# Kernel tuning notes

Measured on AMD Instinct MI355X. Metric: run time of the kernel, lower is better.

Reference implementation:

```python
import jax, jax.numpy as jnp
import numpy as np
from itertools import product

_EPS = 1e-5
N_VOX = 120000
C = 64
B, D, H, Wd = 2, 400, 400, 40  # batch and spatial voxel grid


def _build_rulebook(seed=0):
    """Random unique active voxels + [N,27] submanifold neighbor index table (-1 = inactive)."""
    rng = np.random.default_rng(seed)
    size = B * D * H * Wd
    flat = rng.choice(size, size=N_VOX, replace=False)
    b = flat // (D * H * Wd)
    rem = flat % (D * H * Wd)
    z = rem // (H * Wd)
    rem2 = rem % (H * Wd)
    y = rem2 // Wd
    x = rem2 % Wd
    lut = np.full(size, -1, np.int32)
    lut[flat] = np.arange(N_VOX, dtype=np.int32)
    offs = np.array(list(product([-1, 0, 1], repeat=3)), dtype=np.int64)  # [27,3]
    zz = z[:, None] + offs[None, :, 0]
    yy = y[:, None] + offs[None, :, 1]
    xx = x[:, None] + offs[None, :, 2]
    valid = (zz >= 0) & (zz < D) & (yy >= 0) & (yy < H) & (xx >= 0) & (xx < Wd)
    nf = ((b[:, None] * D + zz) * H + yy) * Wd + xx
    nbr = np.where(valid, lut[np.clip(nf, 0, size - 1)], -1).astype(np.int32)
    return nbr


def setup_inputs() -> dict:
    key = jax.random.key(0)
    ks = jax.random.split(key, 12)
    nbr = jnp.asarray(_build_rulebook())
    return {
        "features": jax.random.normal(ks[0], (N_VOX, C), jnp.float32),
        "W1": jax.random.normal(ks[1], (27, C, C), jnp.float32) * 0.05,
        "g1": jax.random.uniform(ks[2], (C,), jnp.float32, 0.5, 1.5),
        "b1": jax.random.normal(ks[3], (C,), jnp.float32) * 0.1,
        "m1": jax.random.normal(ks[4], (C,), jnp.float32) * 0.1,
        "v1": jax.random.uniform(ks[5], (C,), jnp.float32, 0.5, 1.5),
        "W2": jax.random.normal(ks[6], (27, C, C), jnp.float32) * 0.05,
        "g2": jax.random.uniform(ks[7], (C,), jnp.float32, 0.5, 1.5),
        "b2": jax.random.normal(ks[8], (C,), jnp.float32) * 0.1,
        "m2": jax.random.normal(ks[9], (C,), jnp.float32) * 0.1,
        "v2": jax.random.uniform(ks[10], (C,), jnp.float32, 0.5, 1.5),
        "nbr_idx": nbr,
    }


def _subm_conv(f, nbr, W):
    # gather-GEMM: f [N,Cin], nbr [N,27], W [27,Cin,Cout] -> [N,Cout]
    mask = (nbr >= 0)[:, :, None]
    g = jnp.where(mask, f[jnp.clip(nbr, 0)], jnp.zeros((), f.dtype))  # [N,27,Cin]
    return jnp.einsum('nkc,kcd->nd', g, W)


def _bn(x, g, b, m, v):
    return (x - m) * (g * jax.lax.rsqrt(v + _EPS)) + b


def reference(features, W1, g1, b1, m1, v1, W2, g2, b2, m2, v2, nbr_idx):
    out = _bn(_subm_conv(features, nbr_idx, W1), g1, b1, m1, v1)
    out = jax.nn.relu(out)
    out = _bn(_subm_conv(out, nbr_idx, W2), g2, b2, m2, v2)
    return jax.nn.relu(out + features)
```

## Files before the change

kernel.cpp:

```cpp
#include <hip/hip_runtime.h>

typedef short short8 __attribute__((ext_vector_type(8)));
typedef float f32x4 __attribute__((ext_vector_type(4)));

#define N_VOX 120000
#define C64 64
#define K27 27
#define KC 13
#define TILES 3750
#define CAPT 64
#define LAYER_W 110592
#define CSRB 938
#define PACKB 65
#define FUSEB 938

#define WS_TCNT 0
#define WS_BNP  16384
#define WS_PWC  20480
#define WS_PWT  40960
#define WS_ENTS 524288
#define WS_MIDB (4u << 20)

__device__ __forceinline__ ushort f2bf(float x) {
    uint u = __float_as_uint(x);
    u = (u + 0x7FFFu + ((u >> 16) & 1u)) >> 16;
    return (ushort)u;
}
__device__ __forceinline__ float bf2f(ushort u) {
    return __uint_as_float((uint)u << 16);
}

__global__ __launch_bounds__(256) void prep_csr_kernel(
    const int* __restrict__ nbr,
    const float* __restrict__ W1, const float* __restrict__ W2,
    const float* g1, const float* b1, const float* m1, const float* v1,
    const float* g2, const float* b2, const float* m2, const float* v2,
    int* __restrict__ tcnt, int2* __restrict__ ents,
    ushort* __restrict__ pwt, ushort* __restrict__ pwc,
    float* __restrict__ bnp) {
    if (blockIdx.x < CSRB) {
        __shared__ int cnt_[4];
        const int wv = threadIdx.x >> 6, lane = threadIdx.x & 63;
        const int tile = blockIdx.x * 4 + wv;
        const bool act = tile < TILES;
        if (lane == 0) cnt_[wv] = 0;
        __syncthreads();
        if (act) {
            const int base = tile * (32 * K27);
            for (int e = lane; e < 32 * K27; e += 64) {
                const int k = e % K27;
                if (k == KC) continue;
                const int m = nbr[base + e];
                if (m >= 0) {
                    const int nl = e / K27;
                    int slot = atomicAdd(&cnt_[wv], 1);
                    if (slot < CAPT) ents[tile * CAPT + slot] = make_int2(nl | (k << 8), m);
                }
            }
        }
        __syncthreads();
        if (act && lane == 0) {
            int c = cnt_[wv];
            tcnt[tile] = c > CAPT ? CAPT : c;
        }
    } else {
        int idx = (blockIdx.x - CSRB) * 256 + threadIdx.x;
        const int stride = PACKB * 256;
        for (; idx < 229440; idx += stride) {
            if (idx < 221184) {
                int L = idx / LAYER_W, r = idx % LAYER_W;
                int k = r >> 12, dc = r & 4095, d = dc >> 6, c = dc & 63;
                const float* W = L ? W2 : W1;
                pwt[idx] = f2bf(W[(size_t)k * 4096 + c * 64 + d]);
            } else if (idx < 229376) {
                int j2 = idx - 221184;
                int L = j2 >> 12, q = j2 & 4095;
                int ks = q >> 11, tq = (q >> 9) & 3, ln = (q >> 3) & 63, jj = q & 7;
                int c = ks * 32 + (ln >> 4) * 8 + jj;
                int d = tq * 16 + (ln & 15);
                const float* W = L ? W2 : W1;
                pwc[L * 4096 + q] = f2bf(W[(size_t)KC * 4096 + c * 64 + d]);
            } else {
                int i = idx - 229376;
                float s1 = g1[i] * rsqrtf(v1[i] + 1e-5f);
                bnp[i] = s1; bnp[64 + i] = b1[i] - m1[i] * s1;
                float s2 = g2[i] * rsqrtf(v2[i] + 1e-5f);
                bnp[128 + i] = s2; bnp[192 + i] = b2[i] - m2[i] * s2;
            }
        }
    }
}

template <bool L2P>
__device__ __forceinline__ void fused_core(const float* __restrict__ f,
                                           const ushort* __restrict__ midin,
                                           const ushort* __restrict__ pwc,
                                           const ushort* __restrict__ pwt,
                                           const int* __restrict__ tcnt,
                                           const int2* __restrict__ ents,
                                           const float* __restrict__ bnp,
                                           ushort* __restrict__ midout,
                                           float* __restrict__ fout,
                                           float* exw, int tile) {
    const int lane = threadIdx.x & 63;
    const int r16 = lane & 15, kg = lane >> 4;
    const int n0 = tile * 32;

#pragma unroll
    for (int i = 0; i < 8; ++i) ((f32x4*)exw)[i * 64 + lane] = (f32x4)0.f;

    const short8* B = (const short8*)pwc;
    short8 Bf[2][4];
#pragma unroll
    for (int s = 0; s < 2; ++s)
#pragma unroll
        for (int t = 0; t < 4; ++t) Bf[s][t] = B[(s * 4 + t) * 64 + lane];

    f32x4 acc[2][4];
#pragma unroll
    for (int v = 0; v < 2; ++v)
#pragma unroll
        for (int t = 0; t < 4; ++t) acc[v][t] = (f32x4)0.f;

#pragma unroll
    for (int v = 0; v < 2; ++v) {
        short8 a0, a1;
        if (L2P) {
            const short8* ar = (const short8*)(midin + (size_t)(n0 + v * 16 + r16) * C64);
            a0 = ar[kg];
            a1 = ar[4 + kg];
        } else {
            const float4* ar = (const float4*)(f + (size_t)(n0 + v * 16 + r16) * C64);
            float4 fa = ar[kg * 2], fb = ar[kg * 2 + 1];
            float4 fc = ar[8 + kg * 2], fd = ar[9 + kg * 2];
            a0[0] = f2bf(fa.x); a0[1] = f2bf(fa.y); a0[2] = f2bf(fa.z); a0[3] = f2bf(fa.w);
            a0[4] = f2bf(fb.x); a0[5] = f2bf(fb.y); a0[6] = f2bf(fb.z); a0[7] = f2bf(fb.w);
            a1[0] = f2bf(fc.x); a1[1] = f2bf(fc.y); a1[2] = f2bf(fc.z); a1[3] = f2bf(fc.w);
            a1[4] = f2bf(fd.x); a1[5] = f2bf(fd.y); a1[6] = f2bf(fd.z); a1[7] = f2bf(fd.w);
        }
#pragma unroll
        for (int t = 0; t < 4; ++t) {
            acc[v][t] = __builtin_amdgcn_mfma_f32_16x16x32_bf16(a0, Bf[0][t], acc[v][t], 0, 0, 0);
            acc[v][t] = __builtin_amdgcn_mfma_f32_16x16x32_bf16(a1, Bf[1][t], acc[v][t], 0, 0, 0);
        }
    }

    const int cnt = tcnt[tile];
    for (int p = 0; p < cnt; ++p) {
        int2 e = ents[tile * CAPT + p];
        const int ex = __builtin_amdgcn_readfirstlane(e.x);
        const int m  = __builtin_amdgcn_readfirstlane(e.y);
        const int nl = ex & 255, k = ex >> 8;
        const short8* wr = (const short8*)(pwt + (size_t)k * 4096 + lane * 64);
        float ee0 = 0.f, ee1 = 0.f, ee2 = 0.f, ee3 = 0.f;
        if (L2P) {
            const uint* am = (const uint*)(midin + (size_t)m * C64);
#pragma unroll
            for (int g = 0; g < 8; ++g) {
                short8 w8 = wr[g];
                uint u0 = am[g * 4 + 0], u1 = am[g * 4 + 1];
                uint u2 = am[g * 4 + 2], u3 = am[g * 4 + 3];
                ee0 = fmaf(bf2f((ushort)u0),         bf2f((ushort)w8[0]), ee0);
                ee1 = fmaf(bf2f((ushort)(u0 >> 16)), bf2f((ushort)w8[1]), ee1);
                ee2 = fmaf(bf2f((ushort)u1),         bf2f((ushort)w8[2]), ee2);
                ee3 = fmaf(bf2f((ushort)(u1 >> 16)), bf2f((ushort)w8[3]), ee3);
                ee0 = fmaf(bf2f((ushort)u2),         bf2f((ushort)w8[4]), ee0);
                ee1 = fmaf(bf2f((ushort)(u2 >> 16)), bf2f((ushort)w8[5]), ee1);
                ee2 = fmaf(bf2f((ushort)u3),         bf2f((ushort)w8[6]), ee2);
                ee3 = fmaf(bf2f((ushort)(u3 >> 16)), bf2f((ushort)w8[7]), ee3);
            }
        } else {
            const float4* am = (const float4*)(f + (size_t)m * C64);
#pragma unroll
            for (int g = 0; g < 8; ++g) {
                short8 w8 = wr[g];
                float4 x0 = am[g * 2], x1 = am[g * 2 + 1];
                ee0 = fmaf(x0.x, bf2f((ushort)w8[0]), ee0);
                ee1 = fmaf(x0.y, bf2f((ushort)w8[1]), ee1);
                ee2 = fmaf(x0.z, bf2f((ushort)w8[2]), ee2);
                ee3 = fmaf(x0.w, bf2f((ushort)w8[3]), ee3);
                ee0 = fmaf(x1.x, bf2f((ushort)w8[4]), ee0);
                ee1 = fmaf(x1.y, bf2f((ushort)w8[5]), ee1);
                ee2 = fmaf(x1.z, bf2f((ushort)w8[6]), ee2);
                ee3 = fmaf(x1.w, bf2f((ushort)w8[7]), ee3);
            }
        }
        exw[nl * C64 + lane] += (ee0 + ee1) + (ee2 + ee3);
    }

#pragma unroll
    for (int v = 0; v < 2; ++v)
#pragma unroll
        for (int t = 0; t < 4; ++t)
#pragma unroll
            for (int r = 0; r < 4; ++r)
                exw[(v * 16 + kg * 4 + r) * C64 + t * 16 + r16] += acc[v][t][r];

    const int row = lane >> 1, col0 = (lane & 1) * 32;
    const f32x4* xl = (const f32x4*)(exw + row * C64 + col0);
    const size_t gbase = (size_t)(n0 + row) * C64 + col0;
    if (L2P) {
#pragma unroll
        for (int i = 0; i < 8; ++i) {
            f32x4 x = xl[i];
            float4 s  = *(const float4*)(bnp + col0 + i * 4);
            float4 h  = *(const float4*)(bnp + 64 + col0 + i * 4);
            float4 r4 = *(const float4*)(f + gbase + i * 4);
            float4 o;
            o.x = fmaxf(fmaf(x[0], s.x, h.x) + r4.x, 0.f);
            o.y = fmaxf(fmaf(x[1], s.y, h.y) + r4.y, 0.f);
            o.z = fmaxf(fmaf(x[2], s.z, h.z) + r4.z, 0.f);
            o.w = fmaxf(fmaf(x[3], s.w, h.w) + r4.w, 0.f);
            *(float4*)(fout + gbase + i * 4) = o;
        }
    } else {
#pragma unroll
        for (int i = 0; i < 4; ++i) {
            f32x4 x0 = xl[i * 2], x1 = xl[i * 2 + 1];
            float4 s0 = *(const float4*)(bnp + col0 + i * 8);
            float4 s1 = *(const float4*)(bnp + col0 + i * 8 + 4);
            float4 h0 = *(const float4*)(bnp + 64 + col0 + i * 8);
            float4 h1 = *(const float4*)(bnp + 64 + col0 + i * 8 + 4);
            short8 o;
            o[0] = f2bf(fmaxf(fmaf(x0[0], s0.x, h0.x), 0.f));
            o[1] = f2bf(fmaxf(fmaf(x0[1], s0.y, h0.y), 0.f));
            o[2] = f2bf(fmaxf(fmaf(x0[2], s0.z, h0.z), 0.f));
            o[3] = f2bf(fmaxf(fmaf(x0[3], s0.w, h0.w), 0.f));
            o[4] = f2bf(fmaxf(fmaf(x1[0], s1.x, h1.x), 0.f));
            o[5] = f2bf(fmaxf(fmaf(x1[1], s1.y, h1.y), 0.f));
            o[6] = f2bf(fmaxf(fmaf(x1[2], s1.z, h1.z), 0.f));
            o[7] = f2bf(fmaxf(fmaf(x1[3], s1.w, h1.w), 0.f));
            *(short8*)(midout + gbase + i * 8) = o;
        }
    }
}

__global__ __launch_bounds__(256) void fused_l1_kernel(const float* __restrict__ f,
                                                       const ushort* __restrict__ pwc,
                                                       const ushort* __restrict__ pwt,
                                                       const int* __restrict__ tcnt,
                                                       const int2* __restrict__ ents,
                                                       const float* __restrict__ bnp,
                                                       ushort* __restrict__ midb) {
    __shared__ float ext[4][32 * C64];
    const int wv = threadIdx.x >> 6;
    const int tile = blockIdx.x * 4 + wv;
    if (tile >= TILES) return;
    fused_core<false>(f, nullptr, pwc, pwt, tcnt, ents, bnp, midb, nullptr, ext[wv], tile);
}

__global__ __launch_bounds__(256) void fused_l2_kernel(const float* __restrict__ f,
                                                       const ushort* __restrict__ midb,
                                                       const ushort* __restrict__ pwc,
                                                       const ushort* __restrict__ pwt,
                                                       const int* __restrict__ tcnt,
                                                       const int2* __restrict__ ents,
                                                       const float* __restrict__ bnp,
                                                       float* __restrict__ out) {
    __shared__ float ext[4][32 * C64];
    const int wv = threadIdx.x >> 6;
    const int tile = blockIdx.x * 4 + wv;
    if (tile >= TILES) return;
    fused_core<true>(f, midb, pwc, pwt, tcnt, ents, bnp, nullptr, out, ext[wv], tile);
}

extern "C" void kernel_launch(void* const* d_in, const int* in_sizes, int n_in,
                              void* d_out, int out_size, void* d_ws, size_t ws_size,
                              hipStream_t stream) {
    const float* f   = (const float*)d_in[0];
    const float* W1  = (const float*)d_in[1];
    const float* g1  = (const float*)d_in[2];
    const float* b1  = (const float*)d_in[3];
    const float* m1  = (const float*)d_in[4];
    const float* v1  = (const float*)d_in[5];
    const float* W2  = (const float*)d_in[6];
    const float* g2  = (const float*)d_in[7];
    const float* b2  = (const float*)d_in[8];
    const float* m2  = (const float*)d_in[9];
    const float* v2  = (const float*)d_in[10];
    const int*   nbr = (const int*)d_in[11];
    float* out = (float*)d_out;

    char* ws = (char*)d_ws;
    int*    tcnt = (int*)(ws + WS_TCNT);
    float*  bnp  = (float*)(ws + WS_BNP);
    ushort* pwc  = (ushort*)(ws + WS_PWC);
    ushort* pwt  = (ushort*)(ws + WS_PWT);
    int2*   ents = (int2*)(ws + WS_ENTS);
    ushort* midb = (ushort*)(ws + WS_MIDB);

    prep_csr_kernel<<<CSRB + PACKB, 256, 0, stream>>>(
        nbr, W1, W2, g1, b1, m1, v1, g2, b2, m2, v2, tcnt, ents, pwt, pwc, bnp);

    fused_l1_kernel<<<FUSEB, 256, 0, stream>>>(f, pwc, pwt, tcnt, ents, bnp, midb);
    fused_l2_kernel<<<FUSEB, 256, 0, stream>>>(f, midb, pwc + 4096, pwt + LAYER_W,
                                               tcnt, ents, bnp + 128, out);
}
```

Before: 205.4 us.

## Stage neighbor rows in LDS, precast features to bf16, fp32 coalesced weights

Adds a prep pass that converts the input features to bf16 and repacks the off-center weights as fp32 in a lane-coalesced layout. Each tile now prefetches its neighbor entries and gathered neighbor rows into LDS before the MFMA center-tap step, then processes the extras two at a time. The accumulation buffer is padded to reduce LDS bank conflicts, and launches use one 64-thread wave per block. This targets serialized per-entry global loads and latency in the extras loop, at the cost of an extra bf16 copy of the features, more workspace, and higher register use.

```diff
diff --git a/kernel.cpp b/kernel.cpp
--- a/kernel.cpp
+++ b/kernel.cpp
@@ -9,17 +9,19 @@
 #define KC 13
 #define TILES 3750
 #define CAPT 64
-#define LAYER_W 110592
+#define PAD 66
+#define LAYER_WF 110592
 #define CSRB 938
-#define PACKB 65
-#define FUSEB 938
+#define PACKB 897
+#define FCVTB 3750
 
 #define WS_TCNT 0
 #define WS_BNP  16384
 #define WS_PWC  20480
-#define WS_PWT  40960
-#define WS_ENTS 524288
-#define WS_MIDB (4u << 20)
+#define WS_PWT  65536
+#define WS_ENTS 1048576
+#define WS_FBF  (4u << 20)
+#define WS_MIDB (20u << 20)
 
 __device__ __forceinline__ ushort f2bf(float x) {
     uint u = __float_as_uint(x);
@@ -30,14 +32,14 @@
     return __uint_as_float((uint)u << 16);
 }
 
-__global__ __launch_bounds__(256) void prep_csr_kernel(
-    const int* __restrict__ nbr,
+__global__ __launch_bounds__(256) void prep_kernel(
+    const int* __restrict__ nbr, const float* __restrict__ f,
     const float* __restrict__ W1, const float* __restrict__ W2,
     const float* g1, const float* b1, const float* m1, const float* v1,
     const float* g2, const float* b2, const float* m2, const float* v2,
     int* __restrict__ tcnt, int2* __restrict__ ents,
-    ushort* __restrict__ pwt, ushort* __restrict__ pwc,
-    float* __restrict__ bnp) {
+    float* __restrict__ pwt, ushort* __restrict__ pwc,
+    float* __restrict__ bnp, ushort* __restrict__ fbf) {
     if (blockIdx.x < CSRB) {
         __shared__ int cnt_[4];
         const int wv = threadIdx.x >> 6, lane = threadIdx.x & 63;
@@ -63,52 +65,135 @@
             int c = cnt_[wv];
             tcnt[tile] = c > CAPT ? CAPT : c;
         }
+    } else if (blockIdx.x < CSRB + PACKB) {
+        const int idx = (blockIdx.x - CSRB) * 256 + threadIdx.x;
+        if (idx < 221184) {
+            int L = idx / LAYER_WF, r = idx % LAYER_WF;
+            int k = r >> 12, q = r & 4095;
+            int cc = q >> 9, d = (q >> 3) & 63, cj = q & 7;
+            const float* W = L ? W2 : W1;
+            pwt[idx] = W[(size_t)k * 4096 + (cc * 8 + cj) * 64 + d];
+        } else if (idx < 229376) {
+            int j2 = idx - 221184;
+            int L = j2 >> 12, q = j2 & 4095;
+            int ks = q >> 11, tq = (q >> 9) & 3, ln = (q >> 3) & 63, jj = q & 7;
+            int c = ks * 32 + (ln >> 4) * 8 + jj;
+            int d = tq * 16 + (ln & 15);
+            const float* W = L ? W2 : W1;
+            pwc[L * 4096 + q] = f2bf(W[(size_t)KC * 4096 + c * 64 + d]);
+        } else if (idx < 229440) {
+            int i = idx - 229376;
+            float s1 = g1[i] * rsqrtf(v1[i] + 1e-5f);
+            bnp[i] = s1; bnp[64 + i] = b1[i] - m1[i] * s1;
+            float s2 = g2[i] * rsqrtf(v2[i] + 1e-5f);
+            bnp[128 + i] = s2; bnp[192 + i] = b2[i] - m2[i] * s2;
+        }
     } else {
-        int idx = (blockIdx.x - CSRB) * 256 + threadIdx.x;
-        const int stride = PACKB * 256;
-        for (; idx < 229440; idx += stride) {
-            if (idx < 221184) {
-                int L = idx / LAYER_W, r = idx % LAYER_W;
-                int k = r >> 12, dc = r & 4095, d = dc >> 6, c = dc & 63;
-                const float* W = L ? W2 : W1;
-                pwt[idx] = f2bf(W[(size_t)k * 4096 + c * 64 + d]);
-            } else if (idx < 229376) {
-                int j2 = idx - 221184;
-                int L = j2 >> 12, q = j2 & 4095;
-                int ks = q >> 11, tq = (q >> 9) & 3, ln = (q >> 3) & 63, jj = q & 7;
-                int c = ks * 32 + (ln >> 4) * 8 + jj;
-                int d = tq * 16 + (ln & 15);
-                const float* W = L ? W2 : W1;
-                pwc[L * 4096 + q] = f2bf(W[(size_t)KC * 4096 + c * 64 + d]);
-            } else {
-                int i = idx - 229376;
-                float s1 = g1[i] * rsqrtf(v1[i] + 1e-5f);
-                bnp[i] = s1; bnp[64 + i] = b1[i] - m1[i] * s1;
-                float s2 = g2[i] * rsqrtf(v2[i] + 1e-5f);
-                bnp[128 + i] = s2; bnp[192 + i] = b2[i] - m2[i] * s2;
-            }
-        }
-    }
+        const int i = (blockIdx.x - CSRB - PACKB) * 256 + threadIdx.x;
+        if (i < N_VOX * C64 / 8) {
+            float4 x0 = ((const float4*)f)[i * 2];
+            float4 x1 = ((const float4*)f)[i * 2 + 1];
+            short8 o;
+            o[0] = f2bf(x0.x); o[1] = f2bf(x0.y); o[2] = f2bf(x0.z); o[3] = f2bf(x0.w);
+            o[4] = f2bf(x1.x); o[5] = f2bf(x1.y); o[6] = f2bf(x1.z); o[7] = f2bf(x1.w);
+            ((short8*)fbf)[i] = o;
+        }
+    }
+}
+
+__device__ __forceinline__ void extras_pair2(const float* __restrict__ pwt,
+                                             const ushort* frow, const int2* sents,
+                                             float* ext, int p0, int p1, int lane) {
+    int2 e0 = sents[p0], e1 = sents[p1];
+    const int ex0 = __builtin_amdgcn_readfirstlane(e0.x);
+    const int ex1 = __builtin_amdgcn_readfirstlane(e1.x);
+    const int nl0 = ex0 & 255, k0 = ex0 >> 8;
+    const int nl1 = ex1 & 255, k1 = ex1 >> 8;
+    const float* wk0 = pwt + (size_t)k0 * 4096 + lane * 8;
+    const float* wk1 = pwt + (size_t)k1 * 4096 + lane * 8;
+    float4 wa[16], wb[16];
+#pragma unroll
+    for (int cc = 0; cc < 8; ++cc) {
+        wa[cc * 2]     = *(const float4*)(wk0 + cc * 512);
+        wa[cc * 2 + 1] = *(const float4*)(wk0 + cc * 512 + 4);
+        wb[cc * 2]     = *(const float4*)(wk1 + cc * 512);
+        wb[cc * 2 + 1] = *(const float4*)(wk1 + cc * 512 + 4);
+    }
+    float a0 = 0.f, a1 = 0.f, a2 = 0.f, a3 = 0.f;
+    float b0 = 0.f, b1 = 0.f, b2 = 0.f, b3 = 0.f;
+#pragma unroll
+    for (int cc = 0; cc < 8; ++cc) {
+        short8 fr0 = *(const short8*)(frow + p0 * C64 + cc * 8);
+        short8 fr1 = *(const short8*)(frow + p1 * C64 + cc * 8);
+        float4 x0 = wa[cc * 2], x1 = wa[cc * 2 + 1];
+        float4 y0 = wb[cc * 2], y1 = wb[cc * 2 + 1];
+        a0 = fmaf(bf2f((ushort)fr0[0]), x0.x, a0);
+        a1 = fmaf(bf2f((ushort)fr0[1]), x0.y, a1);
+        a2 = fmaf(bf2f((ushort)fr0[2]), x0.z, a2);
+        a3 = fmaf(bf2f((ushort)fr0[3]), x0.w, a3);
+        a0 = fmaf(bf2f((ushort)fr0[4]), x1.x, a0);
+        a1 = fmaf(bf2f((ushort)fr0[5]), x1.y, a1);
+        a2 = fmaf(bf2f((ushort)fr0[6]), x1.z, a2);
+        a3 = fmaf(bf2f((ushort)fr0[7]), x1.w, a3);
+        b0 = fmaf(bf2f((ushort)fr1[0]), y0.x, b0);
+        b1 = fmaf(bf2f((ushort)fr1[1]), y0.y, b1);
+        b2 = fmaf(bf2f((ushort)fr1[2]), y0.z, b2);
+        b3 = fmaf(bf2f((ushort)fr1[3]), y0.w, b3);
+        b0 = fmaf(bf2f((ushort)fr1[4]), y1.x, b0);
+        b1 = fmaf(bf2f((ushort)fr1[5]), y1.y, b1);
+        b2 = fmaf(bf2f((ushort)fr1[6]), y1.z, b2);
+        b3 = fmaf(bf2f((ushort)fr1[7]), y1.w, b3);
+    }
+    ext[nl0 * PAD + lane] += (a0 + a1) + (a2 + a3);
+    ext[nl1 * PAD + lane] += (b0 + b1) + (b2 + b3);
+}
+
+__device__ __forceinline__ void extras_pair1(const float* __restrict__ pwt,
+                                             const ushort* frow, const int2* sents,
+                                             float* ext, int p, int lane) {
+    int2 e = sents[p];
+    const int ex = __builtin_amdgcn_readfirstlane(e.x);
+    const int nl = ex & 255, k = ex >> 8;
+    const float* wk = pwt + (size_t)k * 4096 + lane * 8;
+    float4 wv[16];
+#pragma unroll
+    for (int cc = 0; cc < 8; ++cc) {
+        wv[cc * 2]     = *(const float4*)(wk + cc * 512);
+        wv[cc * 2 + 1] = *(const float4*)(wk + cc * 512 + 4);
+    }
+    float a0 = 0.f, a1 = 0.f, a2 = 0.f, a3 = 0.f;
+#pragma unroll
+    for (int cc = 0; cc < 8; ++cc) {
+        short8 fr = *(const short8*)(frow + p * C64 + cc * 8);
+        float4 x0 = wv[cc * 2], x1 = wv[cc * 2 + 1];
+        a0 = fmaf(bf2f((ushort)fr[0]), x0.x, a0);
+        a1 = fmaf(bf2f((ushort)fr[1]), x0.y, a1);
+        a2 = fmaf(bf2f((ushort)fr[2]), x0.z, a2);
+        a3 = fmaf(bf2f((ushort)fr[3]), x0.w, a3);
+        a0 = fmaf(bf2f((ushort)fr[4]), x1.x, a0);
+        a1 = fmaf(bf2f((ushort)fr[5]), x1.y, a1);
+        a2 = fmaf(bf2f((ushort)fr[6]), x1.z, a2);
+        a3 = fmaf(bf2f((ushort)fr[7]), x1.w, a3);
+    }
+    ext[nl * PAD + lane] += (a0 + a1) + (a2 + a3);
 }
 
 template <bool L2P>
-__device__ __forceinline__ void fused_core(const float* __restrict__ f,
-                                           const ushort* __restrict__ midin,
+__device__ __forceinline__ void fused_core(const ushort* __restrict__ fin,
+                                           const float* __restrict__ fres,
                                            const ushort* __restrict__ pwc,
-                                           const ushort* __restrict__ pwt,
+                                           const float* __restrict__ pwt,
                                            const int* __restrict__ tcnt,
                                            const int2* __restrict__ ents,
                                            const float* __restrict__ bnp,
                                            ushort* __restrict__ midout,
                                            float* __restrict__ fout,
-                                           float* exw, int tile) {
+                                           float* ext, ushort* frow, int2* sents,
+                                           int tile) {
     const int lane = threadIdx.x & 63;
     const int r16 = lane & 15, kg = lane >> 4;
     const int n0 = tile * 32;
 
-#pragma unroll
-    for (int i = 0; i < 8; ++i) ((f32x4*)exw)[i * 64 + lane] = (f32x4)0.f;
-
     const short8* B = (const short8*)pwc;
     short8 Bf[2][4];
 #pragma unroll
@@ -116,77 +201,51 @@
 #pragma unroll
         for (int t = 0; t < 4; ++t) Bf[s][t] = B[(s * 4 + t) * 64 + lane];
 
+    short8 a[2][2];
+#pragma unroll
+    for (int v = 0; v < 2; ++v) {
+        const short8* ar = (const short8*)(fin + (size_t)(n0 + v * 16 + r16) * C64);
+        a[v][0] = ar[kg];
+        a[v][1] = ar[4 + kg];
+    }
+
+    const int cnt = tcnt[tile];
+    {
+        int2 e = make_int2(0, 0);
+        if (lane < cnt) e = ents[(size_t)tile * CAPT + lane];
+        sents[lane] = e;
+    }
+
+    {
+        const int zr = lane >> 1, zc = (lane & 1) * 32;
+        f32x4* zp = (f32x4*)(ext + zr * PAD + zc);
+#pragma unroll
+        for (int i = 0; i < 8; ++i) zp[i] = (f32x4)0.f;
+    }
+
+#pragma unroll
+    for (int it = 0; it < 8; ++it) {
+        const int base = it * 8;
+        if (base < cnt) {
+            const int p = base + (lane >> 3), j = lane & 7;
+            const int mm = sents[p].y;
+            short8 row = *(const short8*)(fin + (size_t)mm * C64 + j * 8);
+            *(short8*)(frow + p * C64 + j * 8) = row;
+        }
+    }
+
     f32x4 acc[2][4];
 #pragma unroll
     for (int v = 0; v < 2; ++v)
 #pragma unroll
         for (int t = 0; t < 4; ++t) acc[v][t] = (f32x4)0.f;
-
-#pragma unroll
-    for (int v = 0; v < 2; ++v) {
-        short8 a0, a1;
-        if (L2P) {
-            const short8* ar = (const short8*)(midin + (size_t)(n0 + v * 16 + r16) * C64);
-            a0 = ar[kg];
-            a1 = ar[4 + kg];
-        } else {
-            const float4* ar = (const float4*)(f + (size_t)(n0 + v * 16 + r16) * C64);
-            float4 fa = ar[kg * 2], fb = ar[kg * 2 + 1];
-            float4 fc = ar[8 + kg * 2], fd = ar[9 + kg * 2];
-            a0[0] = f2bf(fa.x); a0[1] = f2bf(fa.y); a0[2] = f2bf(fa.z); a0[3] = f2bf(fa.w);
-            a0[4] = f2bf(fb.x); a0[5] = f2bf(fb.y); a0[6] = f2bf(fb.z); a0[7] = f2bf(fb.w);
-            a1[0] = f2bf(fc.x); a1[1] = f2bf(fc.y); a1[2] = f2bf(fc.z); a1[3] = f2bf(fc.w);
-            a1[4] = f2bf(fd.x); a1[5] = f2bf(fd.y); a1[6] = f2bf(fd.z); a1[7] = f2bf(fd.w);
-        }
+#pragma unroll
+    for (int v = 0; v < 2; ++v)
 #pragma unroll
         for (int t = 0; t < 4; ++t) {
-            acc[v][t] = __builtin_amdgcn_mfma_f32_16x16x32_bf16(a0, Bf[0][t], acc[v][t], 0, 0, 0);
-            acc[v][t] = __builtin_amdgcn_mfma_f32_16x16x32_bf16(a1, Bf[1][t], acc[v][t], 0, 0, 0);
-        }
-    }
-
-    const int cnt = tcnt[tile];
-    for (int p = 0; p < cnt; ++p) {
-        int2 e = ents[tile * CAPT + p];
-        const int ex = __builtin_amdgcn_readfirstlane(e.x);
-        const int m  = __builtin_amdgcn_readfirstlane(e.y);
-        const int nl = ex & 255, k = ex >> 8;
-        const short8* wr = (const short8*)(pwt + (size_t)k * 4096 + lane * 64);
-        float ee0 = 0.f, ee1 = 0.f, ee2 = 0.f, ee3 = 0.f;
-        if (L2P) {
-            const uint* am = (const uint*)(midin + (size_t)m * C64);
-#pragma unroll
-            for (int g = 0; g < 8; ++g) {
-                short8 w8 = wr[g];
-                uint u0 = am[g * 4 + 0], u1 = am[g * 4 + 1];
-                uint u2 = am[g * 4 + 2], u3 = am[g * 4 + 3];
-                ee0 = fmaf(bf2f((ushort)u0),         bf2f((ushort)w8[0]), ee0);
-                ee1 = fmaf(bf2f((ushort)(u0 >> 16)), bf2f((ushort)w8[1]), ee1);
-                ee2 = fmaf(bf2f((ushort)u1),         bf2f((ushort)w8[2]), ee2);
-                ee3 = fmaf(bf2f((ushort)(u1 >> 16)), bf2f((ushort)w8[3]), ee3);
-                ee0 = fmaf(bf2f((ushort)u2),         bf2f((ushort)w8[4]), ee0);
-                ee1 = fmaf(bf2f((ushort)(u2 >> 16)), bf2f((ushort)w8[5]), ee1);
-                ee2 = fmaf(bf2f((ushort)u3),         bf2f((ushort)w8[6]), ee2);
-                ee3 = fmaf(bf2f((ushort)(u3 >> 16)), bf2f((ushort)w8[7]), ee3);
-            }
-        } else {
-            const float4* am = (const float4*)(f + (size_t)m * C64);
-#pragma unroll
-            for (int g = 0; g < 8; ++g) {
-                short8 w8 = wr[g];
-                float4 x0 = am[g * 2], x1 = am[g * 2 + 1];
-                ee0 = fmaf(x0.x, bf2f((ushort)w8[0]), ee0);
-                ee1 = fmaf(x0.y, bf2f((ushort)w8[1]), ee1);
-                ee2 = fmaf(x0.z, bf2f((ushort)w8[2]), ee2);
-                ee3 = fmaf(x0.w, bf2f((ushort)w8[3]), ee3);
-                ee0 = fmaf(x1.x, bf2f((ushort)w8[4]), ee0);
-                ee1 = fmaf(x1.y, bf2f((ushort)w8[5]), ee1);
-                ee2 = fmaf(x1.z, bf2f((ushort)w8[6]), ee2);
-                ee3 = fmaf(x1.w, bf2f((ushort)w8[7]), ee3);
-            }
-        }
-        exw[nl * C64 + lane] += (ee0 + ee1) + (ee2 + ee3);
-    }
+            acc[v][t] = __builtin_amdgcn_mfma_f32_16x16x32_bf16(a[v][0], Bf[0][t], acc[v][t], 0, 0, 0);
+            acc[v][t] = __builtin_amdgcn_mfma_f32_16x16x32_bf16(a[v][1], Bf[1][t], acc[v][t], 0, 0, 0);
+        }
 
 #pragma unroll
     for (int v = 0; v < 2; ++v)
@@ -194,10 +253,16 @@
         for (int t = 0; t < 4; ++t)
 #pragma unroll
             for (int r = 0; r < 4; ++r)
-                exw[(v * 16 + kg * 4 + r) * C64 + t * 16 + r16] += acc[v][t][r];
+                ext[(v * 16 + kg * 4 + r) * PAD + t * 16 + r16] += acc[v][t][r];
+
+    int p = 0;
+    for (; p + 1 < cnt; p += 2)
+        extras_pair2(pwt, frow, sents, ext, p, p + 1, lane);
+    if (p < cnt)
+        extras_pair1(pwt, frow, sents, ext, p, lane);
 
     const int row = lane >> 1, col0 = (lane & 1) * 32;
-    const f32x4* xl = (const f32x4*)(exw + row * C64 + col0);
+    const f32x4* xl = (const f32x4*)(ext + row * PAD + col0);
     const size_t gbase = (size_t)(n0 + row) * C64 + col0;
     if (L2P) {
 #pragma unroll
@@ -205,7 +270,7 @@
             f32x4 x = xl[i];
             float4 s  = *(const float4*)(bnp + col0 + i * 4);
             float4 h  = *(const float4*)(bnp + 64 + col0 + i * 4);
-            float4 r4 = *(const float4*)(f + gbase + i * 4);
+            float4 r4 = *(const float4*)(fres + gbase + i * 4);
             float4 o;
             o.x = fmaxf(fmaf(x[0], s.x, h.x) + r4.x, 0.f);
             o.y = fmaxf(fmaf(x[1], s.y, h.y) + r4.y, 0.f);
@@ -235,33 +300,33 @@
     }
 }
 
-__global__ __launch_bounds__(256) void fused_l1_kernel(const float* __restrict__ f,
-                                                       const ushort* __restrict__ pwc,
-                                                       const ushort* __restrict__ pwt,
-                                                       const int* __restrict__ tcnt,
-                                                       const int2* __restrict__ ents,
-                                                       const float* __restrict__ bnp,
-                                                       ushort* __restrict__ midb) {
-    __shared__ float ext[4][32 * C64];
-    const int wv = threadIdx.x >> 6;
-    const int tile = blockIdx.x * 4 + wv;
-    if (tile >= TILES) return;
-    fused_core<false>(f, nullptr, pwc, pwt, tcnt, ents, bnp, midb, nullptr, ext[wv], tile);
-}
-
-__global__ __launch_bounds__(256) void fused_l2_kernel(const float* __restrict__ f,
-                                                       const ushort* __restrict__ midb,
-                                                       const ushort* __restrict__ pwc,
-                                                       const ushort* __restrict__ pwt,
-                                                       const int* __restrict__ tcnt,
-                                                       const int2* __restrict__ ents,
-                                                       const float* __restrict__ bnp,
-                                                       float* __restrict__ out) {
-    __shared__ float ext[4][32 * C64];
-    const int wv = threadIdx.x >> 6;
-    const int tile = blockIdx.x * 4 + wv;
-    if (tile >= TILES) return;
-    fused_core<true>(f, midb, pwc, pwt, tcnt, ents, bnp, nullptr, out, ext[wv], tile);
+__global__ __launch_bounds__(64, 2) void fused_l1_kernel(const ushort* __restrict__ fbf,
+                                                         const ushort* __restrict__ pwc,
+                                                         const float* __restrict__ pwt,
+                                                         const int* __restrict__ tcnt,
+                                                         const int2* __restrict__ ents,
+                                                         const float* __restrict__ bnp,
+                                                         ushort* __restrict__ midb) {
+    __shared__ float  ext[32 * PAD];
+    __shared__ ushort frow[CAPT * C64];
+    __shared__ int2   sents[CAPT];
+    fused_core<false>(fbf, nullptr, pwc, pwt, tcnt, ents, bnp, midb, nullptr,
+                      ext, frow, sents, blockIdx.x);
+}
+
+__global__ __launch_bounds__(64, 2) void fused_l2_kernel(const ushort* __restrict__ midb,
+                                                         const float* __restrict__ f,
+                                                         const ushort* __restrict__ pwc,
+                                                         const float* __restrict__ pwt,
+                                                         const int* __restrict__ tcnt,
+                                                         const int2* __restrict__ ents,
+                                                         const float* __restrict__ bnp,
+                                                         float* __restrict__ out) {
+    __shared__ float  ext[32 * PAD];
+    __shared__ ushort frow[CAPT * C64];
+    __shared__ int2   sents[CAPT];
+    fused_core<true>(midb, f, pwc, pwt, tcnt, ents, bnp, nullptr, out,
+                     ext, frow, sents, blockIdx.x);
 }
 
 extern "C" void kernel_launch(void* const* d_in, const int* in_sizes, int n_in,
@@ -285,14 +350,16 @@
     int*    tcnt = (int*)(ws + WS_TCNT);
     float*  bnp  = (float*)(ws + WS_BNP);
     ushort* pwc  = (ushort*)(ws + WS_PWC);
-    ushort* pwt  = (ushort*)(ws + WS_PWT);
+    float*  pwt  = (float*)(ws + WS_PWT);
     int2*   ents = (int2*)(ws + WS_ENTS);
+    ushort* fbf  = (ushort*)(ws + WS_FBF);
     ushort* midb = (ushort*)(ws + WS_MIDB);
 
-    prep_csr_kernel<<<CSRB + PACKB, 256, 0, stream>>>(
-        nbr, W1, W2, g1, b1, m1, v1, g2, b2, m2, v2, tcnt, ents, pwt, pwc, bnp);
-
-    fused_l1_kernel<<<FUSEB, 256, 0, stream>>>(f, pwc, pwt, tcnt, ents, bnp, midb);
-    fused_l2_kernel<<<FUSEB, 256, 0, stream>>>(f, midb, pwc + 4096, pwt + LAYER_W,
-                                               tcnt, ents, bnp + 128, out);
-}
+    prep_kernel<<<CSRB + PACKB + FCVTB, 256, 0, stream>>>(
+        nbr, f, W1, W2, g1, b1, m1, v1, g2, b2, m2, v2,
+        tcnt, ents, pwt, pwc, bnp, fbf);
+
+    fused_l1_kernel<<<TILES, 64, 0, stream>>>(fbf, pwc, pwt, tcnt, ents, bnp, midb);
+    fused_l2_kernel<<<TILES, 64, 0, stream>>>(midb, f, pwc + 4096, pwt + LAYER_WF,
+                                              tcnt, ents, bnp + 128, out);
+}
```

Measured after the change: 180.9 us. -11.9%, faster.
